# Performance work log

Hardware: AMD Instinct MI355X
Metric: run time of the kernel (lower is better)

The kernel has to match this reference:

```python
import jax, jax.numpy as jnp
import numpy as np

NUM_HEADS = 8

def _mha(x, Wq, Wk, Wv, Wo):
    # x: (..., S, C); standard multi-head self-attention, no bias, no dropout (eval mode)
    C = x.shape[-1]
    dh = C // NUM_HEADS
    lead = x.shape[:-1]
    q = (x @ Wq.T).reshape(*lead, NUM_HEADS, dh)
    k = (x @ Wk.T).reshape(*lead, NUM_HEADS, dh)
    v = (x @ Wv.T).reshape(*lead, NUM_HEADS, dh)
    scores = jnp.einsum('...qhd,...khd->...hqk', q, k) * (dh ** -0.5)
    attn = jax.nn.softmax(scores, axis=-1)
    o = jnp.einsum('...hqk,...khd->...qhd', attn, v).reshape(*lead, C)
    return o @ Wo.T

def _axial_block(xs, Wq_h, Wk_h, Wv_h, Wo_h, Wq_w, Wk_w, Wv_w, Wo_w):
    # xs: (B, C, H, W)
    # height attention: sequence along H, batched over (B, W)
    xh = jnp.transpose(xs, (0, 3, 2, 1))            # (B, W, H, C)
    oh = _mha(xh, Wq_h, Wk_h, Wv_h, Wo_h)           # (B, W, H, C)
    oh = jnp.transpose(oh, (0, 3, 2, 1))            # (B, C, H, W)
    # width attention: sequence along W, batched over (B, H)
    xw = jnp.transpose(xs, (0, 2, 3, 1))            # (B, H, W, C)
    ow = _mha(xw, Wq_w, Wk_w, Wv_w, Wo_w)           # (B, H, W, C)
    ow = jnp.transpose(ow, (0, 3, 1, 2))            # (B, C, H, W)
    return xs + oh + ow

def setup_inputs() -> dict:
    key = jax.random.key(0)
    ks = jax.random.split(key, 9)
    B, C, H, W = 8, 512, 128, 128
    s = C ** -0.5
    xs = jax.random.normal(ks[0], (B, C, H, W), dtype=jnp.float32)
    names = ['Wq_h', 'Wk_h', 'Wv_h', 'Wo_h', 'Wq_w', 'Wk_w', 'Wv_w', 'Wo_w']
    ws = {n: jax.random.normal(k, (C, C), dtype=jnp.float32) * s for n, k in zip(names, ks[1:])}
    return {'xs': xs, **ws}

def reference(xs, Wq_h, Wk_h, Wv_h, Wo_h, Wq_w, Wk_w, Wv_w, Wo_w):
    return _axial_block(xs, Wq_h, Wk_h, Wv_h, Wo_h, Wq_w, Wk_w, Wv_w, Wo_w)
```

## Files before the change

### kernel.cpp

```cpp
#include <hip/hip_runtime.h>

#define CC   512
#define HWT  16384
#define NB   8
#define DH   64
#define SEQ  128
#define C3   1536

typedef __bf16 bf16_t;
typedef __bf16 bf16x8 __attribute__((ext_vector_type(8)));
typedef float  f32x4  __attribute__((ext_vector_type(4)));

#define GLOAD_LDS16(g, l)                                                      \
  __builtin_amdgcn_global_load_lds(                                            \
      (const __attribute__((address_space(1))) void*)(g),                      \
      (__attribute__((address_space(3))) void*)(l), 16, 0, 0)

__global__ __launch_bounds__(256) void prep_w_kernel(const float* __restrict__ W0,
                                                     const float* __restrict__ W1,
                                                     const float* __restrict__ W2,
                                                     const float* __restrict__ W3,
                                                     const float* __restrict__ W4,
                                                     const float* __restrict__ W5,
                                                     const float* __restrict__ W6,
                                                     const float* __restrict__ W7,
                                                     bf16_t* __restrict__ Wb) {
  const float* Wsrc[8] = {W0, W1, W2, W3, W4, W5, W6, W7};
  const int w = blockIdx.y;
  const int i = (blockIdx.x * 256 + threadIdx.x) * 4;
  float4 v = *(const float4*)(Wsrc[w] + i);
  bf16_t* o = Wb + (size_t)w * (CC * CC) + i;
  o[0] = (bf16_t)v.x; o[1] = (bf16_t)v.y; o[2] = (bf16_t)v.z; o[3] = (bf16_t)v.w;
}

__global__ __launch_bounds__(256) void t0_kernel(const float* __restrict__ xs,
                                                 bf16_t* __restrict__ Xt) {
  __shared__ bf16_t T[64 * 72];
  const int hw0 = blockIdx.x * 64, c0 = blockIdx.y * 64;
  const size_t boff = (size_t)blockIdx.z * CC * HWT;
  const int t = threadIdx.x;
  for (int p = 0; p < 4; p++) {
    int job = t + p * 256;
    int c_l = job >> 4, ch = job & 15;
    float4 v = *(const float4*)(xs + boff + (size_t)(c0 + c_l) * HWT + hw0 + ch * 4);
    T[(ch * 4 + 0) * 72 + c_l] = (bf16_t)v.x;
    T[(ch * 4 + 1) * 72 + c_l] = (bf16_t)v.y;
    T[(ch * 4 + 2) * 72 + c_l] = (bf16_t)v.z;
    T[(ch * 4 + 3) * 72 + c_l] = (bf16_t)v.w;
  }
  __syncthreads();
  for (int p = 0; p < 2; p++) {
    int job = t + p * 256;
    int hw_l = job >> 3, ch = job & 7;
    uint4 v = *(const uint4*)&T[hw_l * 72 + ch * 8];
    *(uint4*)(Xt + boff + (size_t)(hw0 + hw_l) * CC + c0 + ch * 8) = v;
  }
}

__global__ __launch_bounds__(256) void gemm_kernel(const bf16_t* __restrict__ A,
                                                   const bf16_t* __restrict__ Wt,
                                                   bf16_t* __restrict__ D,
                                                   int ldD) {
  __shared__ bf16_t As[128 * 32];
  __shared__ bf16_t Ws[128 * 32];
  const int m0 = blockIdx.x * 128, n0 = blockIdx.y * 128;
  const bf16_t* Ab = A + (size_t)blockIdx.z * HWT * CC;
  bf16_t* Db = D + (size_t)blockIdx.z * HWT * (size_t)ldD;
  const int t = threadIdx.x;
  const int lane = t & 63, wv = t >> 6;
  const int wy = wv >> 1, wx = wv & 1;
  const int ln15 = lane & 15, q8 = (lane >> 4) * 8;

  const int seg0 = wv * 2;
  const int srow = lane >> 2;
  const int scol = (lane & 3) * 8;

  f32x4 acc[4][4];
  for (int i = 0; i < 4; i++)
    for (int j = 0; j < 4; j++) acc[i][j] = {0.f, 0.f, 0.f, 0.f};

  for (int kb = 0; kb < 16; kb++) {
    const int kk = kb * 32;
#pragma unroll
    for (int i = 0; i < 2; i++) {
      const int seg = seg0 + i;
      const int row = seg * 16 + srow;
      GLOAD_LDS16(Ab + (size_t)(m0 + row) * CC + kk + scol, &As[seg * 512]);
      GLOAD_LDS16(Wt + (size_t)(n0 + row) * CC + kk + scol, &Ws[seg * 512]);
    }
    __syncthreads();
    bf16x8 af[4], wf[4];
    for (int i = 0; i < 4; i++)
      af[i] = *(const bf16x8*)&As[(wy * 64 + i * 16 + ln15) * 32 + q8];
    for (int j = 0; j < 4; j++)
      wf[j] = *(const bf16x8*)&Ws[(wx * 64 + j * 16 + ln15) * 32 + q8];
    for (int i = 0; i < 4; i++)
      for (int j = 0; j < 4; j++)
        acc[i][j] = __builtin_amdgcn_mfma_f32_16x16x32_bf16(af[i], wf[j], acc[i][j], 0, 0, 0);
    __syncthreads();
  }

  const int qr = (lane >> 4) * 4;
  for (int i = 0; i < 4; i++)
    for (int j = 0; j < 4; j++) {
      const int row = m0 + wy * 64 + i * 16 + qr;
      const int col = n0 + wx * 64 + j * 16 + ln15;
      for (int r = 0; r < 4; r++)
        Db[(size_t)(row + r) * ldD + col] = (bf16_t)acc[i][j][r];
    }
}

__global__ __launch_bounds__(256) void attn_kernel(const bf16_t* __restrict__ Q,
                                                   const bf16_t* __restrict__ K,
                                                   const bf16_t* __restrict__ V,
                                                   bf16_t* __restrict__ O,
                                                   int in_ss, int in_os, int in_bs,
                                                   int out_ss, int out_os, int out_bs) {
  __shared__ bf16_t smem[128 * 72 * 2 + 64 * 136];
  bf16_t* Qs = smem;
  bf16_t* Ks = smem + 128 * 72;
  bf16_t* Vs = smem + 2 * 128 * 72;
  bf16_t* Ps = smem;

  const int o = blockIdx.x, head = blockIdx.y;
  const size_t ibase = (size_t)blockIdx.z * in_bs + (size_t)o * in_os + head * 64;
  const size_t obase = (size_t)blockIdx.z * out_bs + (size_t)o * out_os + head * 64;
  const int t = threadIdx.x, lane = t & 63, wv = t >> 6;
  const int ln15 = lane & 15, q = lane >> 4;

  for (int p = 0; p < 4; p++) {
    int job = t + p * 256;
    int s = job >> 3, ch = job & 7;
    uint4 qv = *(const uint4*)(Q + ibase + (size_t)s * in_ss + ch * 8);
    uint4 kv = *(const uint4*)(K + ibase + (size_t)s * in_ss + ch * 8);
    *(uint4*)&Qs[s * 72 + ch * 8] = qv;
    *(uint4*)&Ks[s * 72 + ch * 8] = kv;
  }
  for (int p = 0; p < 4; p++) {
    int job = t + p * 256;
    int s = job >> 3, ch = job & 7;
    uint4 vv = *(const uint4*)(V + ibase + (size_t)s * in_ss + ch * 8);
    const bf16_t* e = (const bf16_t*)&vv;
    for (int jj = 0; jj < 8; jj++) Vs[(ch * 8 + jj) * 136 + s] = e[jj];
  }
  __syncthreads();

  f32x4 sacc[2][8];
  for (int i = 0; i < 2; i++)
    for (int j = 0; j < 8; j++) sacc[i][j] = {0.f, 0.f, 0.f, 0.f};
  for (int ks = 0; ks < 2; ks++) {
    bf16x8 qf[2], kf[8];
    for (int i = 0; i < 2; i++)
      qf[i] = *(const bf16x8*)&Qs[(wv * 32 + i * 16 + ln15) * 72 + ks * 32 + q * 8];
    for (int j = 0; j < 8; j++)
      kf[j] = *(const bf16x8*)&Ks[(j * 16 + ln15) * 72 + ks * 32 + q * 8];
    for (int i = 0; i < 2; i++)
      for (int j = 0; j < 8; j++)
        sacc[i][j] = __builtin_amdgcn_mfma_f32_16x16x32_bf16(qf[i], kf[j], sacc[i][j], 0, 0, 0);
  }
  __syncthreads();

  const float scale = 0.125f;
  float linv[2][4];
  for (int i = 0; i < 2; i++)
    for (int r = 0; r < 4; r++) {
      float m = -1e30f;
      for (int j = 0; j < 8; j++) m = fmaxf(m, sacc[i][j][r]);
      for (int d = 1; d < 16; d <<= 1) m = fmaxf(m, __shfl_xor(m, d));
      m *= scale;
      float sum = 0.f;
      for (int j = 0; j < 8; j++) {
        float pv = __expf(sacc[i][j][r] * scale - m);
        sacc[i][j][r] = pv;
        sum += pv;
      }
      for (int d = 1; d < 16; d <<= 1) sum += __shfl_xor(sum, d);
      linv[i][r] = 1.f / sum;
    }
  for (int i = 0; i < 2; i++)
    for (int j = 0; j < 8; j++)
      for (int r = 0; r < 4; r++)
        Ps[(wv * 32 + i * 16 + q * 4 + r) * 136 + j * 16 + ln15] = (bf16_t)sacc[i][j][r];
  __syncthreads();

  f32x4 oacc[2][4];
  for (int i = 0; i < 2; i++)
    for (int j = 0; j < 4; j++) oacc[i][j] = {0.f, 0.f, 0.f, 0.f};
  for (int ks = 0; ks < 4; ks++) {
    bf16x8 pf[2], vf[4];
    for (int i = 0; i < 2; i++)
      pf[i] = *(const bf16x8*)&Ps[(wv * 32 + i * 16 + ln15) * 136 + ks * 32 + q * 8];
    for (int j = 0; j < 4; j++)
      vf[j] = *(const bf16x8*)&Vs[(j * 16 + ln15) * 136 + ks * 32 + q * 8];
    for (int i = 0; i < 2; i++)
      for (int j = 0; j < 4; j++)
        oacc[i][j] = __builtin_amdgcn_mfma_f32_16x16x32_bf16(pf[i], vf[j], oacc[i][j], 0, 0, 0);
  }
  for (int i = 0; i < 2; i++)
    for (int j = 0; j < 4; j++)
      for (int r = 0; r < 4; r++) {
        const int s = wv * 32 + i * 16 + q * 4 + r;
        const int d = j * 16 + ln15;
        O[obase + (size_t)s * out_ss + d] = (bf16_t)(oacc[i][j][r] * linv[i][r]);
      }
}

__global__ __launch_bounds__(256) void final_add_kernel(const float* __restrict__ xs,
                                                        const bf16_t* __restrict__ OH,
                                                        const bf16_t* __restrict__ OW,
                                                        float* __restrict__ out) {
  __shared__ float TF[64 * 65];
  const int hw0 = blockIdx.x * 64, c0 = blockIdx.y * 64;
  const size_t boff = (size_t)blockIdx.z * CC * HWT;
  const int t = threadIdx.x;
  for (int p = 0; p < 2; p++) {
    int job = t + p * 256;
    int hw_l = job >> 3, ch = job & 7;
    size_t off = boff + (size_t)(hw0 + hw_l) * CC + c0 + ch * 8;
    bf16x8 a = *(const bf16x8*)(OH + off);
    bf16x8 b = *(const bf16x8*)(OW + off);
    for (int jj = 0; jj < 8; jj++)
      TF[(ch * 8 + jj) * 65 + hw_l] = (float)a[jj] + (float)b[jj];
  }
  __syncthreads();
  for (int p = 0; p < 4; p++) {
    int job = t + p * 256;
    int c_l = job >> 4, ch = job & 15;
    size_t off = boff + (size_t)(c0 + c_l) * HWT + hw0 + ch * 4;
    float4 xv = *(const float4*)(xs + off);
    float4 ov;
    ov.x = xv.x + TF[c_l * 65 + ch * 4 + 0];
    ov.y = xv.y + TF[c_l * 65 + ch * 4 + 1];
    ov.z = xv.z + TF[c_l * 65 + ch * 4 + 2];
    ov.w = xv.w + TF[c_l * 65 + ch * 4 + 3];
    *(float4*)(out + off) = ov;
  }
}

extern "C" void kernel_launch(void* const* d_in, const int* in_sizes, int n_in,
                              void* d_out, int out_size, void* d_ws, size_t ws_size,
                              hipStream_t stream) {
  const float* xs = (const float*)d_in[0];
  float* out = (float*)d_out;

  bf16_t* Wb = (bf16_t*)d_ws;
  const size_t wbytes = (size_t)8 * CC * CC * sizeof(bf16_t);
  bf16_t* wsb = Wb + (size_t)8 * CC * CC;

  const size_t pb = (size_t)HWT * CC;
  size_t avail = (ws_size > wbytes) ? (ws_size - wbytes) : 0;
  int chunkB = (int)(avail / (6 * pb * sizeof(bf16_t)));
  if (chunkB > NB) chunkB = NB;
  if (chunkB < 1) chunkB = 1;
  const size_t R = (size_t)chunkB * pb;
  bf16_t* Xt  = wsb;
  bf16_t* QKV = wsb + R;
  bf16_t* Ab  = wsb + 4 * R;
  bf16_t* OH  = wsb + 5 * R;

  prep_w_kernel<<<dim3(CC * CC / 1024, 8), 256, 0, stream>>>(
      (const float*)d_in[1], (const float*)d_in[2], (const float*)d_in[3],
      (const float*)d_in[4], (const float*)d_in[5], (const float*)d_in[6],
      (const float*)d_in[7], (const float*)d_in[8], Wb);
  const bf16_t* Wqkv_h = Wb + 0 * (size_t)CC * CC;
  const bf16_t* Wo_h   = Wb + 3 * (size_t)CC * CC;
  const bf16_t* Wqkv_w = Wb + 4 * (size_t)CC * CC;
  const bf16_t* Wo_w   = Wb + 7 * (size_t)CC * CC;

  for (int b0 = 0; b0 < NB; b0 += chunkB) {
    const int cb = (NB - b0 < chunkB) ? (NB - b0) : chunkB;
    const float* xsc = xs + (size_t)b0 * pb;
    float* outc = out + (size_t)b0 * pb;
    dim3 gT(HWT / 64, CC / 64, cb);
    dim3 gQKV(HWT / 128, C3 / 128, cb);
    dim3 gO(HWT / 128, CC / 128, cb);
    dim3 gA(128, 8, cb);
    dim3 blk(256);

    t0_kernel<<<gT, blk, 0, stream>>>(xsc, Xt);
    gemm_kernel<<<gQKV, blk, 0, stream>>>(Xt, Wqkv_h, QKV, C3);
    attn_kernel<<<gA, blk, 0, stream>>>(QKV, QKV + 512, QKV + 1024, Ab,
                                        128 * C3, C3, HWT * C3,
                                        128 * CC, CC, HWT * CC);
    gemm_kernel<<<gO, blk, 0, stream>>>(Ab, Wo_h, OH, CC);
    gemm_kernel<<<gQKV, blk, 0, stream>>>(Xt, Wqkv_w, QKV, C3);
    attn_kernel<<<gA, blk, 0, stream>>>(QKV, QKV + 512, QKV + 1024, Ab,
                                        C3, 128 * C3, HWT * C3,
                                        CC, 128 * CC, HWT * CC);
    gemm_kernel<<<gO, blk, 0, stream>>>(Ab, Wo_w, Xt, CC);
    final_add_kernel<<<gT, blk, 0, stream>>>(xsc, OH, Xt, outc);
  }
}
```

Baseline: 1.629 ms.

## Replace 128x128 GEMM with pipelined 256x256 tile kernel using double-buffered LDS

Swaps the simple 128x128 bf16 GEMM for a 512-thread 256x256-tile kernel that double-buffers 64-wide K slices in LDS. It interleaves async global-to-LDS loads with MFMA phases using explicit vmcnt waits and barriers, XOR-swizzles LDS columns to cut bank conflicts, and remaps blocks for L2 locality. The aim is to raise arithmetic intensity and hide global memory latency in the projection GEMMs. In exchange it uses 128KB of LDS per block and many accumulator registers, and its hand-tuned waitcnt/barrier schedule is fragile.

```diff
diff --git a/kernel.cpp b/kernel.cpp
--- a/kernel.cpp
+++ b/kernel.cpp
@@ -15,6 +15,17 @@
   __builtin_amdgcn_global_load_lds(                                            \
       (const __attribute__((address_space(1))) void*)(g),                      \
       (__attribute__((address_space(3))) void*)(l), 16, 0, 0)
+
+#define WAITV4() asm volatile("s_waitcnt vmcnt(4)" ::: "memory")
+#define WAITV0() asm volatile("s_waitcnt vmcnt(0)" ::: "memory")
+#define LGKM0()  asm volatile("s_waitcnt lgkmcnt(0)" ::: "memory")
+#define BARX()                                                                 \
+  {                                                                            \
+    asm volatile("" ::: "memory");                                             \
+    __builtin_amdgcn_s_barrier();                                              \
+    asm volatile("" ::: "memory");                                             \
+  }
+#define MFMA(d, x, y) d = __builtin_amdgcn_mfma_f32_16x16x32_bf16(x, y, d, 0, 0, 0)
 
 __global__ __launch_bounds__(256) void prep_w_kernel(const float* __restrict__ W0,
                                                      const float* __restrict__ W1,
@@ -57,57 +68,247 @@
   }
 }
 
-__global__ __launch_bounds__(256) void gemm_kernel(const bf16_t* __restrict__ A,
-                                                   const bf16_t* __restrict__ Wt,
-                                                   bf16_t* __restrict__ D,
-                                                   int ldD) {
-  __shared__ bf16_t As[128 * 32];
-  __shared__ bf16_t Ws[128 * 32];
-  const int m0 = blockIdx.x * 128, n0 = blockIdx.y * 128;
+__global__ __launch_bounds__(512, 2) void gemm256_kernel(const bf16_t* __restrict__ A,
+                                                         const bf16_t* __restrict__ Wt,
+                                                         bf16_t* __restrict__ D,
+                                                         int ldD) {
+  __shared__ bf16_t smem[65536];
+  bf16_t* As = smem;
+  bf16_t* Bs = smem + 32768;
+
+  const int flat = blockIdx.x + 64 * blockIdx.y;
+  const int cpx = (64 * gridDim.y) >> 3;
+  const int swz = (flat & 7) * cpx + (flat >> 3);
+  const int m0 = (swz & 63) << 8;
+  const int n0 = (swz >> 6) << 8;
   const bf16_t* Ab = A + (size_t)blockIdx.z * HWT * CC;
   bf16_t* Db = D + (size_t)blockIdx.z * HWT * (size_t)ldD;
+
   const int t = threadIdx.x;
   const int lane = t & 63, wv = t >> 6;
-  const int wy = wv >> 1, wx = wv & 1;
+  const int wm = wv >> 2, wn = wv & 3;
   const int ln15 = lane & 15, q8 = (lane >> 4) * 8;
-
-  const int seg0 = wv * 2;
-  const int srow = lane >> 2;
-  const int scol = (lane & 3) * 8;
-
-  f32x4 acc[4][4];
-  for (int i = 0; i < 4; i++)
-    for (int j = 0; j < 4; j++) acc[i][j] = {0.f, 0.f, 0.f, 0.f};
-
-  for (int kb = 0; kb < 16; kb++) {
-    const int kk = kb * 32;
-#pragma unroll
-    for (int i = 0; i < 2; i++) {
-      const int seg = seg0 + i;
-      const int row = seg * 16 + srow;
-      GLOAD_LDS16(Ab + (size_t)(m0 + row) * CC + kk + scol, &As[seg * 512]);
-      GLOAD_LDS16(Wt + (size_t)(n0 + row) * CC + kk + scol, &Ws[seg * 512]);
-    }
-    __syncthreads();
-    bf16x8 af[4], wf[4];
-    for (int i = 0; i < 4; i++)
-      af[i] = *(const bf16x8*)&As[(wy * 64 + i * 16 + ln15) * 32 + q8];
-    for (int j = 0; j < 4; j++)
-      wf[j] = *(const bf16x8*)&Ws[(wx * 64 + j * 16 + ln15) * 32 + q8];
-    for (int i = 0; i < 4; i++)
-      for (int j = 0; j < 4; j++)
-        acc[i][j] = __builtin_amdgcn_mfma_f32_16x16x32_bf16(af[i], wf[j], acc[i][j], 0, 0, 0);
-    __syncthreads();
+  const int xr = ((ln15 >> 2) & 3) << 3;
+  const int cA = q8 ^ xr;
+  const int srow = t >> 3;
+  const int scol = ((t & 7) * 8) ^ (((t >> 5) & 3) << 3);
+
+#define FRAGLD(dst, tile, row, ks)                                             \
+  dst = *(const bf16x8*)((tile) + (row) * 64 + cA + (ks) * 32)
+
+#define STAGE_HALF(src, ldsHalf)                                               \
+  {                                                                            \
+    GLOAD_LDS16((src) + (size_t)srow * CC + scol, (ldsHalf) + wv * 512);       \
+    GLOAD_LDS16((src) + (size_t)(64 + srow) * CC + scol,                       \
+                (ldsHalf) + 4096 + wv * 512);                                  \
+  }
+#define STAGE_A(kt, half)                                                      \
+  STAGE_HALF(Ab + (size_t)(m0 + (half) * 128) * CC + (kt) * 64,                \
+             As + ((kt) & 1) * 16384 + (half) * 8192)
+#define STAGE_B(kt, half)                                                      \
+  STAGE_HALF(Wt + (size_t)(n0 + (half) * 128) * CC + (kt) * 64,                \
+             Bs + ((kt) & 1) * 16384 + (half) * 8192)
+
+  f32x4 acc[8][4];
+#pragma unroll
+  for (int f = 0; f < 8; f++)
+#pragma unroll
+    for (int g = 0; g < 4; g++) acc[f][g] = {0.f, 0.f, 0.f, 0.f};
+  bf16x8 a[4][2], b0[2][2], b1[2][2];
+
+  STAGE_A(0, 0); STAGE_A(0, 1);
+  STAGE_B(0, 0); STAGE_B(0, 1);
+  STAGE_B(1, 0); STAGE_B(1, 1);
+  WAITV4();
+  BARX();
+
+#pragma unroll 1
+  for (int i = 0; i < 4; i++) {
+    const int kt0 = 2 * i;
+    const bool last = (i == 3);
+    const bf16_t* At0 = As;
+    const bf16_t* Bt0 = Bs;
+    const bf16_t* At1 = As + 16384;
+    const bf16_t* Bt1 = Bs + 16384;
+
+#pragma unroll
+    for (int f = 0; f < 4; f++) {
+      const int row = wm * 128 + f * 16 + ln15;
+      FRAGLD(a[f][0], At0, row, 0);
+      FRAGLD(a[f][1], At0, row, 1);
+    }
+#pragma unroll
+    for (int g = 0; g < 2; g++) {
+      const int row = wn * 64 + g * 16 + ln15;
+      FRAGLD(b0[g][0], Bt0, row, 0);
+      FRAGLD(b0[g][1], Bt0, row, 1);
+    }
+    STAGE_A(kt0 + 1, 0);
+    BARX(); LGKM0();
+    __builtin_amdgcn_s_setprio(1);
+#pragma unroll
+    for (int f = 0; f < 4; f++)
+#pragma unroll
+      for (int g = 0; g < 2; g++) {
+        MFMA(acc[f][g], a[f][0], b0[g][0]);
+        MFMA(acc[f][g], a[f][1], b0[g][1]);
+      }
+    __builtin_amdgcn_s_setprio(0);
+    BARX();
+
+#pragma unroll
+    for (int g = 0; g < 2; g++) {
+      const int row = wn * 64 + (g + 2) * 16 + ln15;
+      FRAGLD(b1[g][0], Bt0, row, 0);
+      FRAGLD(b1[g][1], Bt0, row, 1);
+    }
+    STAGE_A(kt0 + 1, 1);
+    BARX(); LGKM0();
+    __builtin_amdgcn_s_setprio(1);
+#pragma unroll
+    for (int f = 0; f < 4; f++)
+#pragma unroll
+      for (int g = 0; g < 2; g++) {
+        MFMA(acc[f][g + 2], a[f][0], b1[g][0]);
+        MFMA(acc[f][g + 2], a[f][1], b1[g][1]);
+      }
+    __builtin_amdgcn_s_setprio(0);
+    BARX();
+
+#pragma unroll
+    for (int f = 0; f < 4; f++) {
+      const int row = wm * 128 + (f + 4) * 16 + ln15;
+      FRAGLD(a[f][0], At0, row, 0);
+      FRAGLD(a[f][1], At0, row, 1);
+    }
+    if (!last) STAGE_B(kt0 + 2, 0);
+    BARX(); LGKM0();
+    __builtin_amdgcn_s_setprio(1);
+#pragma unroll
+    for (int f = 0; f < 4; f++)
+#pragma unroll
+      for (int g = 0; g < 2; g++) {
+        MFMA(acc[f + 4][g + 2], a[f][0], b1[g][0]);
+        MFMA(acc[f + 4][g + 2], a[f][1], b1[g][1]);
+      }
+    __builtin_amdgcn_s_setprio(0);
+    BARX();
+
+    if (!last) {
+      STAGE_B(kt0 + 2, 1);
+      WAITV4();
+    } else {
+      WAITV0();
+    }
+    BARX();
+    __builtin_amdgcn_s_setprio(1);
+#pragma unroll
+    for (int f = 0; f < 4; f++)
+#pragma unroll
+      for (int g = 0; g < 2; g++) {
+        MFMA(acc[f + 4][g], a[f][0], b0[g][0]);
+        MFMA(acc[f + 4][g], a[f][1], b0[g][1]);
+      }
+    __builtin_amdgcn_s_setprio(0);
+    BARX();
+
+#pragma unroll
+    for (int f = 0; f < 4; f++) {
+      const int row = wm * 128 + f * 16 + ln15;
+      FRAGLD(a[f][0], At1, row, 0);
+      FRAGLD(a[f][1], At1, row, 1);
+    }
+#pragma unroll
+    for (int g = 0; g < 2; g++) {
+      const int row = wn * 64 + g * 16 + ln15;
+      FRAGLD(b0[g][0], Bt1, row, 0);
+      FRAGLD(b0[g][1], Bt1, row, 1);
+    }
+    if (!last) STAGE_A(kt0 + 2, 0);
+    BARX(); LGKM0();
+    __builtin_amdgcn_s_setprio(1);
+#pragma unroll
+    for (int f = 0; f < 4; f++)
+#pragma unroll
+      for (int g = 0; g < 2; g++) {
+        MFMA(acc[f][g], a[f][0], b0[g][0]);
+        MFMA(acc[f][g], a[f][1], b0[g][1]);
+      }
+    __builtin_amdgcn_s_setprio(0);
+    BARX();
+
+#pragma unroll
+    for (int g = 0; g < 2; g++) {
+      const int row = wn * 64 + (g + 2) * 16 + ln15;
+      FRAGLD(b1[g][0], Bt1, row, 0);
+      FRAGLD(b1[g][1], Bt1, row, 1);
+    }
+    if (!last) STAGE_A(kt0 + 2, 1);
+    BARX(); LGKM0();
+    __builtin_amdgcn_s_setprio(1);
+#pragma unroll
+    for (int f = 0; f < 4; f++)
+#pragma unroll
+      for (int g = 0; g < 2; g++) {
+        MFMA(acc[f][g + 2], a[f][0], b1[g][0]);
+        MFMA(acc[f][g + 2], a[f][1], b1[g][1]);
+      }
+    __builtin_amdgcn_s_setprio(0);
+    BARX();
+
+#pragma unroll
+    for (int f = 0; f < 4; f++) {
+      const int row = wm * 128 + (f + 4) * 16 + ln15;
+      FRAGLD(a[f][0], At1, row, 0);
+      FRAGLD(a[f][1], At1, row, 1);
+    }
+    if (!last) STAGE_B(kt0 + 3, 0);
+    BARX(); LGKM0();
+    __builtin_amdgcn_s_setprio(1);
+#pragma unroll
+    for (int f = 0; f < 4; f++)
+#pragma unroll
+      for (int g = 0; g < 2; g++) {
+        MFMA(acc[f + 4][g + 2], a[f][0], b1[g][0]);
+        MFMA(acc[f + 4][g + 2], a[f][1], b1[g][1]);
+      }
+    __builtin_amdgcn_s_setprio(0);
+    BARX();
+
+    if (!last) {
+      STAGE_B(kt0 + 3, 1);
+      WAITV4();
+    }
+    BARX();
+    __builtin_amdgcn_s_setprio(1);
+#pragma unroll
+    for (int f = 0; f < 4; f++)
+#pragma unroll
+      for (int g = 0; g < 2; g++) {
+        MFMA(acc[f + 4][g], a[f][0], b0[g][0]);
+        MFMA(acc[f + 4][g], a[f][1], b0[g][1]);
+      }
+    __builtin_amdgcn_s_setprio(0);
+    BARX();
   }
 
   const int qr = (lane >> 4) * 4;
-  for (int i = 0; i < 4; i++)
-    for (int j = 0; j < 4; j++) {
-      const int row = m0 + wy * 64 + i * 16 + qr;
-      const int col = n0 + wx * 64 + j * 16 + ln15;
+  const int crow = m0 + wm * 128;
+  const int ccol = n0 + wn * 64;
+#pragma unroll
+  for (int f = 0; f < 8; f++)
+#pragma unroll
+    for (int g = 0; g < 4; g++) {
+      const int row = crow + f * 16 + qr;
+      const int col = ccol + g * 16 + ln15;
+#pragma unroll
       for (int r = 0; r < 4; r++)
-        Db[(size_t)(row + r) * ldD + col] = (bf16_t)acc[i][j][r];
-    }
+        Db[(size_t)(row + r) * ldD + col] = (bf16_t)acc[f][g][r];
+    }
+#undef FRAGLD
+#undef STAGE_HALF
+#undef STAGE_A
+#undef STAGE_B
 }
 
 __global__ __launch_bounds__(256) void attn_kernel(const bf16_t* __restrict__ Q,
@@ -272,22 +473,22 @@
     const float* xsc = xs + (size_t)b0 * pb;
     float* outc = out + (size_t)b0 * pb;
     dim3 gT(HWT / 64, CC / 64, cb);
-    dim3 gQKV(HWT / 128, C3 / 128, cb);
-    dim3 gO(HWT / 128, CC / 128, cb);
+    dim3 gQKV(HWT / 256, C3 / 256, cb);
+    dim3 gO(HWT / 256, CC / 256, cb);
     dim3 gA(128, 8, cb);
-    dim3 blk(256);
+    dim3 blk(256), blk5(512);
 
     t0_kernel<<<gT, blk, 0, stream>>>(xsc, Xt);
-    gemm_kernel<<<gQKV, blk, 0, stream>>>(Xt, Wqkv_h, QKV, C3);
+    gemm256_kernel<<<gQKV, blk5, 0, stream>>>(Xt, Wqkv_h, QKV, C3);
     attn_kernel<<<gA, blk, 0, stream>>>(QKV, QKV + 512, QKV + 1024, Ab,
                                         128 * C3, C3, HWT * C3,
                                         128 * CC, CC, HWT * CC);
-    gemm_kernel<<<gO, blk, 0, stream>>>(Ab, Wo_h, OH, CC);
-    gemm_kernel<<<gQKV, blk, 0, stream>>>(Xt, Wqkv_w, QKV, C3);
+    gemm256_kernel<<<gO, blk5, 0, stream>>>(Ab, Wo_h, OH, CC);
+    gemm256_kernel<<<gQKV, blk5, 0, stream>>>(Xt, Wqkv_w, QKV, C3);
     attn_kernel<<<gA, blk, 0, stream>>>(QKV, QKV + 512, QKV + 1024, Ab,
                                         C3, 128 * C3, HWT * C3,
                                         CC, 128 * CC, HWT * CC);
-    gemm_kernel<<<gO, blk, 0, stream>>>(Ab, Wo_w, Xt, CC);
+    gemm256_kernel<<<gO, blk5, 0, stream>>>(Ab, Wo_w, Xt, CC);
     final_add_kernel<<<gT, blk, 0, stream>>>(xsc, OH, Xt, outc);
   }
 }
```

New measurement: 1.627 ms. No clear change (-0.2%).
